# Kernel optimization log

Measured on AMD Instinct MI355X. Metric: run time of the kernel, lower is better.

Reference implementation:

```python
import jax, jax.numpy as jnp
import numpy as np

B, T, D, UNITS = 64, 1024, 512, 1024

def setup_inputs() -> dict:
    key = jax.random.key(0)
    ks = jax.random.split(key, 8)
    s = lambda fan_in: 1.0 / np.sqrt(fan_in)
    return {
        "features": jax.random.normal(ks[0], (B, T, D), dtype=jnp.float32),
        "hidden": jax.random.normal(ks[1], (B, D), dtype=jnp.float32),
        "W1_w": jax.random.normal(ks[2], (D, UNITS), dtype=jnp.float32) * s(D),
        "W1_b": jnp.zeros((UNITS,), dtype=jnp.float32),
        "W2_w": jax.random.normal(ks[3], (D, UNITS), dtype=jnp.float32) * s(D),
        "W2_b": jnp.zeros((UNITS,), dtype=jnp.float32),
        "V_w": jax.random.normal(ks[4], (UNITS, 1), dtype=jnp.float32) * s(UNITS),
        "V_b": jnp.zeros((1,), dtype=jnp.float32),
    }

def reference(features, hidden, W1_w, W1_b, W2_w, W2_b, V_w, V_b):
    # features: [B,T,D], hidden: [B,D]
    proj_f = jnp.einsum('btd,du->btu', features, W1_w) + W1_b          # [B,T,U]
    proj_h = (hidden @ W2_w + W2_b)[:, None, :]                        # [B,1,U]
    score = jnp.tanh(proj_f + proj_h)                                  # [B,T,U]
    logits = jnp.einsum('btu,uo->bto', score, V_w) + V_b               # [B,T,1]
    attention_weights = jax.nn.softmax(logits, axis=1)                 # [B,T,1]
    context_vector = jnp.sum(attention_weights * features, axis=1)     # [B,D]
    return context_vector, attention_weights
```

## Files before the change

### kernel.cpp

```cpp
#include <hip/hip_runtime.h>
#include <math.h>

#define B_ 64
#define T_ 1024
#define D_ 512
#define U_ 1024

typedef __bf16 bf16x8 __attribute__((ext_vector_type(8)));
typedef float f32x16 __attribute__((ext_vector_type(16)));
typedef unsigned int u32;

__device__ __forceinline__ float tanh_from_x2(float x2) {
    const float xc = __builtin_amdgcn_fmed3f(x2, -18.f, 18.f);
    const float e  = __expf(xc);
    const float r  = __builtin_amdgcn_rcpf(e + 1.0f);
    return fmaf(-2.0f, r, 1.0f);
}

__device__ __forceinline__ u32 f2bf_pk(float lo, float hi) {
    u32 a = __float_as_uint(lo) + 0x8000u;
    u32 b = __float_as_uint(hi) + 0x8000u;
    return __builtin_amdgcn_perm(b, a, 0x07060302u);
}

__global__ __launch_bounds__(256) void prep_kernel(
    const float* __restrict__ W1, const float* __restrict__ hidden,
    const float* __restrict__ W2, const float* __restrict__ W2b,
    const float* __restrict__ W1b,
    unsigned short* __restrict__ W1F, float* __restrict__ ph,
    float* __restrict__ ctx0) {
    if (blockIdx.x < 256) {
        const int gid  = blockIdx.x * 256 + threadIdx.x;
        const int lane = gid & 63;
        const int frag = gid >> 6;
        const int ks = frag & 1;
        const int kt = (frag >> 1) & 15;
        const int ut = frag >> 5;
        const int u  = ut * 32 + (lane & 31);
        const int k0 = kt * 32 + ks * 16 + (lane >> 5) * 8;
        float f[8];
#pragma unroll
        for (int j = 0; j < 8; ++j) f[j] = W1[(size_t)(k0 + j) * U_ + u];
        uint4 w;
        w.x = f2bf_pk(f[0], f[1]);
        w.y = f2bf_pk(f[2], f[3]);
        w.z = f2bf_pk(f[4], f[5]);
        w.w = f2bf_pk(f[6], f[7]);
        *(uint4*)&W1F[(size_t)gid * 8] = w;
    } else {
        const int bx = blockIdx.x - 256;
        const int zi = bx * 256 + (int)threadIdx.x;
        if (zi < B_ * D_) ctx0[zi] = 0.f;
        const int u  = (bx & 3) * 256 + threadIdx.x;
        const int b  = bx >> 2;
        const float* h = hidden + b * D_;
        float acc = 0.f;
#pragma unroll 8
        for (int d = 0; d < D_; ++d) acc = fmaf(h[d], W2[(size_t)d * U_ + u], acc);
        ph[b * U_ + u] = acc + W2b[u] + W1b[u];
    }
}

__global__ __launch_bounds__(256, 2) void logits_mfma_kernel(
    const float* __restrict__ feat,
    const unsigned short* __restrict__ W1F,
    const float* __restrict__ ph,
    const float* __restrict__ Vw,
    float* __restrict__ lpart) {
    __shared__ __align__(16) char As[65536];

    const int tid  = threadIdx.x;
    const int gx   = blockIdx.x;
    const int uh   = gx & 1;
    const int tt   = gx >> 1;
    const int b    = blockIdx.y;
    const int t0   = tt * 64;
    const int lane = tid & 63;
    const int widx = tid >> 6;
    const int l31 = lane & 31, g = lane >> 5;

    {
        const int r  = tid >> 2;
        const int s0 = tid & 3;
        const float* src = feat + ((size_t)(b * T_ + t0 + r)) * D_;
        const int xr = (r >> 2) & 3;
#pragma unroll
        for (int i = 0; i < 16; ++i) {
            const int s = s0 + 4 * i;
            const float4 v0 = *(const float4*)(src + s * 8);
            const float4 v1 = *(const float4*)(src + s * 8 + 4);
            uint4 w;
            w.x = f2bf_pk(v0.x, v0.y);
            w.y = f2bf_pk(v0.z, v0.w);
            w.z = f2bf_pk(v1.x, v1.y);
            w.w = f2bf_pk(v1.z, v1.w);
            const int panel = s >> 2, q = s & 3;
            *(uint4*)&As[panel * 4096 + r * 64 + (q ^ xr) * 16] = w;
        }
    }
    __syncthreads();

    const char* bfbase = (const char*)W1F +
                         (size_t)((uh * 16 + widx * 4)) * 32768 + lane * 16;

    f32x16 acc[2][4];
    bf16x8 b0[8], b1[8];

    auto loadB = [&](bf16x8* dst, int kt) {
#pragma unroll
        for (int nt = 0; nt < 4; ++nt)
#pragma unroll
            for (int ks = 0; ks < 2; ++ks)
                dst[nt * 2 + ks] =
                    *(const bf16x8*)(bfbase + nt * 32768 + (kt * 2 + ks) * 1024);
    };

    auto computeStep = [&](int kt, const bf16x8* bfr) {
        bf16x8 af[2][2];
#pragma unroll
        for (int ks = 0; ks < 2; ++ks)
#pragma unroll
            for (int mt = 0; mt < 2; ++mt) {
                const int rr = mt * 32 + l31;
                const int q  = (2 * ks + g) ^ ((rr >> 2) & 3);
                af[ks][mt] = *(const bf16x8*)&As[kt * 4096 + rr * 64 + q * 16];
            }
        __builtin_amdgcn_s_setprio(1);
#pragma unroll
        for (int ks = 0; ks < 2; ++ks)
#pragma unroll
            for (int mt = 0; mt < 2; ++mt)
#pragma unroll
                for (int nt = 0; nt < 4; ++nt)
                    acc[mt][nt] = __builtin_amdgcn_mfma_f32_32x32x16_bf16(
                        af[ks][mt], bfr[nt * 2 + ks], acc[mt][nt], 0, 0, 0);
        __builtin_amdgcn_s_setprio(0);
    };

#pragma unroll
    for (int mt = 0; mt < 2; ++mt)
#pragma unroll
        for (int nt = 0; nt < 4; ++nt) acc[mt][nt] = (f32x16)(0.f);

    loadB(b0, 0);
    for (int kt = 0; kt < 16; kt += 2) {
        loadB(b1, kt + 1);
        computeStep(kt, b0);
        if (kt + 2 < 16) loadB(b0, kt + 2);
        computeStep(kt + 1, b1);
    }

    float v[32];
#pragma unroll
    for (int i = 0; i < 32; ++i) v[i] = 0.f;

#pragma unroll
    for (int nt = 0; nt < 4; ++nt) {
        const int u = uh * 512 + widx * 128 + nt * 32 + l31;
        const float phv2 = 2.0f * ph[b * U_ + u];
        const float vw   = Vw[u];
#pragma unroll
        for (int mt = 0; mt < 2; ++mt)
#pragma unroll
            for (int r = 0; r < 16; ++r) {
                const float th =
                    tanh_from_x2(fmaf(2.0f, acc[mt][nt][r], phv2));
                v[mt * 16 + r] = fmaf(vw, th, v[mt * 16 + r]);
            }
    }

#pragma unroll
    for (int s = 0; s < 5; ++s) {
        const int pb = 1 << s;
        const bool hi = (l31 & pb) != 0;
#pragma unroll
        for (int j = 0; j < (16 >> s); ++j) {
            const float a = v[2 * j];
            const float c = v[2 * j + 1];
            const float keep = hi ? c : a;
            const float send = hi ? a : c;
            v[j] = keep + __shfl_xor(send, pb);
        }
    }

    const int src = ((lane & 3) | (((lane >> 3) & 3) << 2) |
                     (((lane >> 5) & 1) << 4)) + 32 * ((lane >> 2) & 1);
    const float out = __shfl(v[0], src);
    lpart[((size_t)(uh * 4 + widx)) * (B_ * T_) + (size_t)b * T_ + t0 + lane] =
        out;
}

__global__ __launch_bounds__(512) void ctx_kernel(
    const float* __restrict__ feat, const float* __restrict__ lpart,
    float* __restrict__ attn, float* __restrict__ ctx_out) {
    const int b   = blockIdx.y;
    const int seg = blockIdx.x;
    const int tid = threadIdx.x;
    __shared__ float wls[1024];
    __shared__ float redm[8];
    __shared__ float reds[8];

    float v[2];
    float mx = -3.4e38f;
#pragma unroll
    for (int j = 0; j < 2; ++j) {
        const int t = b * T_ + tid + 512 * j;
        float s0 = 0.f, s1 = 0.f;
#pragma unroll
        for (int sl = 0; sl < 4; ++sl) {
            s0 += lpart[(size_t)(2 * sl) * (B_ * T_) + t];
            s1 += lpart[(size_t)(2 * sl + 1) * (B_ * T_) + t];
        }
        v[j] = s0 + s1;
        mx = fmaxf(mx, v[j]);
    }
#pragma unroll
    for (int off = 32; off > 0; off >>= 1) mx = fmaxf(mx, __shfl_xor(mx, off));
    if ((tid & 63) == 0) redm[tid >> 6] = mx;
    __syncthreads();
    mx = fmaxf(fmaxf(fmaxf(redm[0], redm[1]), fmaxf(redm[2], redm[3])),
               fmaxf(fmaxf(redm[4], redm[5]), fmaxf(redm[6], redm[7])));
    float s = 0.f;
#pragma unroll
    for (int j = 0; j < 2; ++j) {
        v[j] = __expf(v[j] - mx);
        s += v[j];
    }
#pragma unroll
    for (int off = 32; off > 0; off >>= 1) s += __shfl_xor(s, off);
    if ((tid & 63) == 0) reds[tid >> 6] = s;
    __syncthreads();
    s = ((reds[0] + reds[1]) + (reds[2] + reds[3])) +
        ((reds[4] + reds[5]) + (reds[6] + reds[7]));
    const float inv = 1.0f / s;
    wls[tid]       = v[0] * inv;
    wls[tid + 512] = v[1] * inv;
    __syncthreads();

    if (tid < 128) attn[b * T_ + seg * 128 + tid] = wls[seg * 128 + tid];

    const int q  = tid >> 7;
    const int d4 = (tid & 127) * 4;
    const int t0 = seg * 128 + q * 32;
    const float* fb = feat + ((size_t)(b * T_ + t0)) * D_ + d4;
    const float* wb = &wls[t0];
    float4 acc = {0.f, 0.f, 0.f, 0.f};
#pragma unroll 4
    for (int t = 0; t < 32; ++t) {
        const float w  = wb[t];
        const float4 f = *(const float4*)&fb[(size_t)t * D_];
        acc.x = fmaf(w, f.x, acc.x);
        acc.y = fmaf(w, f.y, acc.y);
        acc.z = fmaf(w, f.z, acc.z);
        acc.w = fmaf(w, f.w, acc.w);
    }
    float* dst = ctx_out + b * D_ + d4;
    atomicAdd(dst + 0, acc.x);
    atomicAdd(dst + 1, acc.y);
    atomicAdd(dst + 2, acc.z);
    atomicAdd(dst + 3, acc.w);
}

extern "C" void kernel_launch(void* const* d_in, const int* in_sizes, int n_in,
                              void* d_out, int out_size, void* d_ws, size_t ws_size,
                              hipStream_t stream) {
    const float* feat   = (const float*)d_in[0];
    const float* hidden = (const float*)d_in[1];
    const float* W1w    = (const float*)d_in[2];
    const float* W1b    = (const float*)d_in[3];
    const float* W2w    = (const float*)d_in[4];
    const float* W2b    = (const float*)d_in[5];
    const float* Vw     = (const float*)d_in[6];

    float* out_ctx  = (float*)d_out;
    float* out_attn = out_ctx + B_ * D_;

    unsigned short* W1F = (unsigned short*)d_ws;
    float* ph     = (float*)(W1F + (size_t)U_ * D_);
    float* lpart  = ph + B_ * U_;

    prep_kernel<<<512, 256, 0, stream>>>(W1w, hidden, W2w, W2b, W1b, W1F, ph,
                                         out_ctx);
    logits_mfma_kernel<<<dim3(32, B_), 256, 0, stream>>>(feat, W1F, ph, Vw,
                                                         lpart);
    ctx_kernel<<<dim3(8, B_), 512, 0, stream>>>(feat, lpart, out_attn, out_ctx);
}
```

Measured before the change: 312.1 us.

## Make logits kernel persistent over time tiles with double-buffered feature staging

Each block now walks 8 tiles of 32 timesteps instead of one tile of 64, with the next tile's features loaded into registers and written to a second LDS buffer while MFMAs run on the current one. The grid shrinks from 32x64 to 8x64 blocks, and per-wave M tile drops from 64 to 32 rows. The aim is to hide global load and bf16 conversion latency behind compute and hoist the ph/Vw loads. The cost is that W1 fragments are reloaded from global/L2 every tile with half the reuse per load, fewer blocks are available for occupancy, and there is an extra barrier per tile.

New measurement: 739.5 us. +136.9%, slower.

```diff
diff --git a/kernel.cpp b/kernel.cpp
--- a/kernel.cpp
+++ b/kernel.cpp
@@ -5,6 +5,7 @@
 #define T_ 1024
 #define D_ 512
 #define U_ 1024
+#define NTILE 8
 
 typedef __bf16 bf16x8 __attribute__((ext_vector_type(8)));
 typedef float f32x16 __attribute__((ext_vector_type(16)));
@@ -67,45 +68,60 @@
     const float* __restrict__ ph,
     const float* __restrict__ Vw,
     float* __restrict__ lpart) {
-    __shared__ __align__(16) char As[65536];
+    __shared__ __align__(16) char As[2][32768];
 
     const int tid  = threadIdx.x;
     const int gx   = blockIdx.x;
     const int uh   = gx & 1;
-    const int tt   = gx >> 1;
+    const int tg   = gx >> 1;
     const int b    = blockIdx.y;
-    const int t0   = tt * 64;
     const int lane = tid & 63;
     const int widx = tid >> 6;
     const int l31 = lane & 31, g = lane >> 5;
 
-    {
-        const int r  = tid >> 2;
-        const int s0 = tid & 3;
-        const float* src = feat + ((size_t)(b * T_ + t0 + r)) * D_;
-        const int xr = (r >> 2) & 3;
-#pragma unroll
-        for (int i = 0; i < 16; ++i) {
-            const int s = s0 + 4 * i;
-            const float4 v0 = *(const float4*)(src + s * 8);
-            const float4 v1 = *(const float4*)(src + s * 8 + 4);
+    const int r  = tid >> 3;
+    const int s0 = tid & 7;
+    const int xr = (r >> 2) & 3;
+    const float* asrc = feat + ((size_t)(b * T_ + tg * (32 * NTILE) + r)) * D_;
+
+    const char* bfbase = (const char*)W1F +
+                         (size_t)(uh * 16 + widx * 4) * 32768 + lane * 16;
+
+    float phv2[4], vwv[4];
+#pragma unroll
+    for (int nt = 0; nt < 4; ++nt) {
+        const int u = uh * 512 + widx * 128 + nt * 32 + l31;
+        phv2[nt] = 2.0f * ph[b * U_ + u];
+        vwv[nt]  = Vw[u];
+    }
+
+    float4 sr[8];
+    auto issueA = [&](int i, int h) {
+#pragma unroll
+        for (int j = 0; j < 4; ++j) {
+            const int s = s0 + 8 * (4 * h + j);
+            const float* p = asrc + (size_t)i * 32 * D_ + s * 8;
+            sr[2 * j]     = *(const float4*)p;
+            sr[2 * j + 1] = *(const float4*)(p + 4);
+        }
+    };
+    auto writeA = [&](int i, int h) {
+        char* dbuf = As[i & 1];
+#pragma unroll
+        for (int j = 0; j < 4; ++j) {
+            const int s = s0 + 8 * (4 * h + j);
             uint4 w;
-            w.x = f2bf_pk(v0.x, v0.y);
-            w.y = f2bf_pk(v0.z, v0.w);
-            w.z = f2bf_pk(v1.x, v1.y);
-            w.w = f2bf_pk(v1.z, v1.w);
+            w.x = f2bf_pk(sr[2 * j].x, sr[2 * j].y);
+            w.y = f2bf_pk(sr[2 * j].z, sr[2 * j].w);
+            w.z = f2bf_pk(sr[2 * j + 1].x, sr[2 * j + 1].y);
+            w.w = f2bf_pk(sr[2 * j + 1].z, sr[2 * j + 1].w);
             const int panel = s >> 2, q = s & 3;
-            *(uint4*)&As[panel * 4096 + r * 64 + (q ^ xr) * 16] = w;
-        }
-    }
-    __syncthreads();
-
-    const char* bfbase = (const char*)W1F +
-                         (size_t)((uh * 16 + widx * 4)) * 32768 + lane * 16;
-
-    f32x16 acc[2][4];
-    bf16x8 b0[8], b1[8];
-
+            *(uint4*)&dbuf[panel * 2048 + r * 64 + (q ^ xr) * 16] = w;
+        }
+    };
+
+    f32x16 acc[4];
+    bf16x8 b0f[8], b1f[8];
     auto loadB = [&](bf16x8* dst, int kt) {
 #pragma unroll
         for (int nt = 0; nt < 4; ++nt)
@@ -114,80 +130,89 @@
                 dst[nt * 2 + ks] =
                     *(const bf16x8*)(bfbase + nt * 32768 + (kt * 2 + ks) * 1024);
     };
-
-    auto computeStep = [&](int kt, const bf16x8* bfr) {
-        bf16x8 af[2][2];
+    auto computeStep = [&](const char* abuf, int kt, const bf16x8* bfr) {
+        bf16x8 af[2];
+#pragma unroll
+        for (int ks = 0; ks < 2; ++ks) {
+            const int q = (2 * ks + g) ^ ((l31 >> 2) & 3);
+            af[ks] = *(const bf16x8*)&abuf[kt * 2048 + l31 * 64 + q * 16];
+        }
+        __builtin_amdgcn_s_setprio(1);
 #pragma unroll
         for (int ks = 0; ks < 2; ++ks)
 #pragma unroll
-            for (int mt = 0; mt < 2; ++mt) {
-                const int rr = mt * 32 + l31;
-                const int q  = (2 * ks + g) ^ ((rr >> 2) & 3);
-                af[ks][mt] = *(const bf16x8*)&As[kt * 4096 + rr * 64 + q * 16];
-            }
-        __builtin_amdgcn_s_setprio(1);
-#pragma unroll
-        for (int ks = 0; ks < 2; ++ks)
-#pragma unroll
-            for (int mt = 0; mt < 2; ++mt)
-#pragma unroll
-                for (int nt = 0; nt < 4; ++nt)
-                    acc[mt][nt] = __builtin_amdgcn_mfma_f32_32x32x16_bf16(
-                        af[ks][mt], bfr[nt * 2 + ks], acc[mt][nt], 0, 0, 0);
+            for (int nt = 0; nt < 4; ++nt)
+                acc[nt] = __builtin_amdgcn_mfma_f32_32x32x16_bf16(
+                    af[ks], bfr[nt * 2 + ks], acc[nt], 0, 0, 0);
         __builtin_amdgcn_s_setprio(0);
     };
 
 #pragma unroll
-    for (int mt = 0; mt < 2; ++mt)
-#pragma unroll
-        for (int nt = 0; nt < 4; ++nt) acc[mt][nt] = (f32x16)(0.f);
-
-    loadB(b0, 0);
-    for (int kt = 0; kt < 16; kt += 2) {
-        loadB(b1, kt + 1);
-        computeStep(kt, b0);
-        if (kt + 2 < 16) loadB(b0, kt + 2);
-        computeStep(kt + 1, b1);
-    }
-
-    float v[32];
-#pragma unroll
-    for (int i = 0; i < 32; ++i) v[i] = 0.f;
-
-#pragma unroll
-    for (int nt = 0; nt < 4; ++nt) {
-        const int u = uh * 512 + widx * 128 + nt * 32 + l31;
-        const float phv2 = 2.0f * ph[b * U_ + u];
-        const float vw   = Vw[u];
-#pragma unroll
-        for (int mt = 0; mt < 2; ++mt)
-#pragma unroll
-            for (int r = 0; r < 16; ++r) {
-                const float th =
-                    tanh_from_x2(fmaf(2.0f, acc[mt][nt][r], phv2));
-                v[mt * 16 + r] = fmaf(vw, th, v[mt * 16 + r]);
+    for (int nt = 0; nt < 4; ++nt) acc[nt] = (f32x16)(0.f);
+
+    issueA(0, 0); writeA(0, 0);
+    issueA(0, 1); writeA(0, 1);
+    __syncthreads();
+
+    for (int i = 0; i < NTILE; ++i) {
+        const char* abuf = As[i & 1];
+        const bool pf = (i + 1 < NTILE);
+
+        if (pf) issueA(i + 1, 0);
+        loadB(b0f, 0);
+#pragma unroll
+        for (int kt = 0; kt < 8; kt += 2) {
+            loadB(b1f, kt + 1);
+            computeStep(abuf, kt, b0f);
+            loadB(b0f, kt + 2);
+            computeStep(abuf, kt + 1, b1f);
+        }
+        if (pf) { writeA(i + 1, 0); issueA(i + 1, 1); }
+#pragma unroll
+        for (int kt = 8; kt < 16; kt += 2) {
+            loadB(b1f, kt + 1);
+            computeStep(abuf, kt, b0f);
+            if (kt + 2 < 16) loadB(b0f, kt + 2);
+            computeStep(abuf, kt + 1, b1f);
+        }
+        if (pf) writeA(i + 1, 1);
+
+        float v[16];
+#pragma unroll
+        for (int k = 0; k < 16; ++k) v[k] = 0.f;
+#pragma unroll
+        for (int nt = 0; nt < 4; ++nt)
+#pragma unroll
+            for (int rr = 0; rr < 16; ++rr)
+                v[rr] = fmaf(vwv[nt],
+                             tanh_from_x2(fmaf(2.0f, acc[nt][rr], phv2[nt])),
+                             v[rr]);
+#pragma unroll
+        for (int nt = 0; nt < 4; ++nt) acc[nt] = (f32x16)(0.f);
+
+#pragma unroll
+        for (int st = 0; st < 4; ++st) {
+            const int pb = 1 << st;
+            const bool hi = (l31 & pb) != 0;
+#pragma unroll
+            for (int j = 0; j < (8 >> st); ++j) {
+                const float a = v[2 * j];
+                const float c = v[2 * j + 1];
+                const float keep = hi ? c : a;
+                const float send = hi ? a : c;
+                v[j] = keep + __shfl_xor(send, pb);
             }
-    }
-
-#pragma unroll
-    for (int s = 0; s < 5; ++s) {
-        const int pb = 1 << s;
-        const bool hi = (l31 & pb) != 0;
-#pragma unroll
-        for (int j = 0; j < (16 >> s); ++j) {
-            const float a = v[2 * j];
-            const float c = v[2 * j + 1];
-            const float keep = hi ? c : a;
-            const float send = hi ? a : c;
-            v[j] = keep + __shfl_xor(send, pb);
-        }
-    }
-
-    const int src = ((lane & 3) | (((lane >> 3) & 3) << 2) |
-                     (((lane >> 5) & 1) << 4)) + 32 * ((lane >> 2) & 1);
-    const float out = __shfl(v[0], src);
-    lpart[((size_t)(uh * 4 + widx)) * (B_ * T_) + (size_t)b * T_ + t0 + lane] =
-        out;
+        }
+        v[0] += __shfl_xor(v[0], 16);
+
+        const int srcl = ((lane & 3) | (((lane >> 3) & 3) << 2)) +
+                         32 * ((lane >> 2) & 1);
+        const float out = __shfl(v[0], srcl);
+        if (lane < 32)
+            lpart[(size_t)(uh * 4 + widx) * (B_ * T_) + (size_t)b * T_ +
+                  tg * (32 * NTILE) + i * 32 + lane] = out;
+        __syncthreads();
+    }
 }
 
 __global__ __launch_bounds__(512) void ctx_kernel(
@@ -281,7 +306,7 @@
 
     prep_kernel<<<512, 256, 0, stream>>>(W1w, hidden, W2w, W2b, W1b, W1F, ph,
                                          out_ctx);
-    logits_mfma_kernel<<<dim3(32, B_), 256, 0, stream>>>(feat, W1F, ph, Vw,
-                                                         lpart);
+    logits_mfma_kernel<<<dim3(8, B_), 256, 0, stream>>>(feat, W1F, ph, Vw,
+                                                        lpart);
     ctx_kernel<<<dim3(8, B_), 512, 0, stream>>>(feat, lpart, out_attn, out_ctx);
 }
```

## Split context reduction over D slices instead of T segments, drop atomics

Applied to the files above, without the earlier changes.

The context kernel now gives each block a 64-wide slice of D covering all 1024 timesteps. Eight thread groups each handle 128 timesteps, and their partial sums are combined through shared memory, then written directly. This removes the float atomicAdds and the zero-initialisation of the output in prep_kernel. The trade-off is that each thread now does scalar 4-byte loads in a 128-step serial loop instead of float4 loads over 32 steps, which may lower memory-level parallelism when streaming the features.

Result: faster. 303.8 us (-2.7%).

```diff
diff --git a/kernel.cpp b/kernel.cpp
--- a/kernel.cpp
+++ b/kernel.cpp
@@ -27,8 +27,7 @@
     const float* __restrict__ W1, const float* __restrict__ hidden,
     const float* __restrict__ W2, const float* __restrict__ W2b,
     const float* __restrict__ W1b,
-    unsigned short* __restrict__ W1F, float* __restrict__ ph,
-    float* __restrict__ ctx0) {
+    unsigned short* __restrict__ W1F, float* __restrict__ ph) {
     if (blockIdx.x < 256) {
         const int gid  = blockIdx.x * 256 + threadIdx.x;
         const int lane = gid & 63;
@@ -49,8 +48,6 @@
         *(uint4*)&W1F[(size_t)gid * 8] = w;
     } else {
         const int bx = blockIdx.x - 256;
-        const int zi = bx * 256 + (int)threadIdx.x;
-        if (zi < B_ * D_) ctx0[zi] = 0.f;
         const int u  = (bx & 3) * 256 + threadIdx.x;
         const int b  = bx >> 2;
         const float* h = hidden + b * D_;
@@ -194,11 +191,12 @@
     const float* __restrict__ feat, const float* __restrict__ lpart,
     float* __restrict__ attn, float* __restrict__ ctx_out) {
     const int b   = blockIdx.y;
-    const int seg = blockIdx.x;
+    const int ds  = blockIdx.x;
     const int tid = threadIdx.x;
     __shared__ float wls[1024];
     __shared__ float redm[8];
     __shared__ float reds[8];
+    __shared__ float cpart[8][64];
 
     float v[2];
     float mx = -3.4e38f;
@@ -237,28 +235,28 @@
     wls[tid + 512] = v[1] * inv;
     __syncthreads();
 
-    if (tid < 128) attn[b * T_ + seg * 128 + tid] = wls[seg * 128 + tid];
-
-    const int q  = tid >> 7;
-    const int d4 = (tid & 127) * 4;
-    const int t0 = seg * 128 + q * 32;
-    const float* fb = feat + ((size_t)(b * T_ + t0)) * D_ + d4;
-    const float* wb = &wls[t0];
-    float4 acc = {0.f, 0.f, 0.f, 0.f};
+    if (ds == 0) {
+        attn[b * T_ + tid]       = wls[tid];
+        attn[b * T_ + tid + 512] = wls[tid + 512];
+    }
+
+    const int tc = tid >> 6;
+    const int dl = tid & 63;
+    const float* fb =
+        feat + ((size_t)(b * T_ + tc * 128)) * D_ + ds * 64 + dl;
+    const float* wb = &wls[tc * 128];
+    float acc = 0.f;
 #pragma unroll 4
-    for (int t = 0; t < 32; ++t) {
-        const float w  = wb[t];
-        const float4 f = *(const float4*)&fb[(size_t)t * D_];
-        acc.x = fmaf(w, f.x, acc.x);
-        acc.y = fmaf(w, f.y, acc.y);
-        acc.z = fmaf(w, f.z, acc.z);
-        acc.w = fmaf(w, f.w, acc.w);
-    }
-    float* dst = ctx_out + b * D_ + d4;
-    atomicAdd(dst + 0, acc.x);
-    atomicAdd(dst + 1, acc.y);
-    atomicAdd(dst + 2, acc.z);
-    atomicAdd(dst + 3, acc.w);
+    for (int t = 0; t < 128; ++t)
+        acc = fmaf(wb[t], fb[(size_t)t * D_], acc);
+    cpart[tc][dl] = acc;
+    __syncthreads();
+    if (tid < 64) {
+        float cs = 0.f;
+#pragma unroll
+        for (int k = 0; k < 8; ++k) cs += cpart[k][tid];
+        ctx_out[b * D_ + ds * 64 + tid] = cs;
+    }
 }
 
 extern "C" void kernel_launch(void* const* d_in, const int* in_sizes, int n_in,
@@ -279,8 +277,7 @@
     float* ph     = (float*)(W1F + (size_t)U_ * D_);
     float* lpart  = ph + B_ * U_;
 
-    prep_kernel<<<512, 256, 0, stream>>>(W1w, hidden, W2w, W2b, W1b, W1F, ph,
-                                         out_ctx);
+    prep_kernel<<<512, 256, 0, stream>>>(W1w, hidden, W2w, W2b, W1b, W1F, ph);
     logits_mfma_kernel<<<dim3(32, B_), 256, 0, stream>>>(feat, W1F, ph, Vw,
                                                          lpart);
     ctx_kernel<<<dim3(8, B_), 512, 0, stream>>>(feat, lpart, out_attn, out_ctx);
```
